# Kernel optimization log

Hardware: AMD Instinct MI355X
Metric: run time of the kernel (lower is better)

Reference implementation:

```python
import jax, jax.numpy as jnp
import numpy as np

N_NODES = 50000
NEG_SLOPE = 0.2


def _gat_conv(x, edge_index, W, att_src, att_dst, bias, heads, out_ch, concat):
    """PyG-style GATConv (add_self_loops=True, negative_slope=0.2).
    x: [N, F_in], edge_index: [2, E] (row=src, row=dst), W: [F_in, heads*out_ch],
    att_src/att_dst: [heads, out_ch], bias: [heads*out_ch] or [out_ch]."""
    N = x.shape[0]
    # add self-loops
    loops = jnp.arange(N, dtype=edge_index.dtype)
    src = jnp.concatenate([edge_index[0], loops])
    dst = jnp.concatenate([edge_index[1], loops])

    h = (x @ W).reshape(N, heads, out_ch)                 # [N, H, C]
    a_src = jnp.einsum('nhc,hc->nh', h, att_src)          # [N, H]
    a_dst = jnp.einsum('nhc,hc->nh', h, att_dst)          # [N, H]

    e = a_src[src] + a_dst[dst]                           # [E', H]
    e = jnp.where(e >= 0, e, NEG_SLOPE * e)               # leaky_relu

    # segment softmax over incoming edges of each dst node
    e_max = jax.ops.segment_max(e, dst, num_segments=N)   # [N, H]
    e_max = jnp.where(jnp.isfinite(e_max), e_max, 0.0)
    ex = jnp.exp(e - e_max[dst])                          # [E', H]
    denom = jax.ops.segment_sum(ex, dst, num_segments=N)  # [N, H]
    alpha = ex / (denom[dst] + 1e-16)                     # [E', H]

    msg = alpha[:, :, None] * h[src]                      # [E', H, C]
    out = jax.ops.segment_sum(msg, dst, num_segments=N)   # [N, H, C]

    if concat:
        out = out.reshape(N, heads * out_ch)
    else:
        out = out.mean(axis=1)
    return out + bias


def setup_inputs() -> dict:
    key = jax.random.key(0)
    ks = jax.random.split(key, 12)
    F_in, hid, H1, C, H2 = 512, 8, 8, 40, 1
    x = jax.random.normal(ks[0], (N_NODES, F_in), dtype=jnp.float32)
    edge_index = jax.random.randint(ks[1], (2, 1600000), 0, N_NODES, dtype=jnp.int64)
    s1 = 1.0 / np.sqrt(F_in)
    s2 = 1.0 / np.sqrt(hid * H1)
    return {
        'x': x,
        'edge_index': edge_index,
        'W1': jax.random.normal(ks[2], (F_in, H1 * hid), dtype=jnp.float32) * s1,
        'att_src1': jax.random.normal(ks[3], (H1, hid), dtype=jnp.float32) * s2,
        'att_dst1': jax.random.normal(ks[4], (H1, hid), dtype=jnp.float32) * s2,
        'b1': jnp.zeros((H1 * hid,), dtype=jnp.float32),
        'W2': jax.random.normal(ks[5], (H1 * hid, H2 * C), dtype=jnp.float32) * s2,
        'att_src2': jax.random.normal(ks[6], (H2, C), dtype=jnp.float32) * 0.15,
        'att_dst2': jax.random.normal(ks[7], (H2, C), dtype=jnp.float32) * 0.15,
        'b2': jnp.zeros((C,), dtype=jnp.float32),
    }


def reference(x, edge_index, W1, att_src1, att_dst1, b1, W2, att_src2, att_dst2, b2):
    # eval mode: dropout is identity
    h = _gat_conv(x, edge_index, W1, att_src1, att_dst1, b1, heads=8, out_ch=8, concat=True)
    h = jax.nn.relu(h)
    h = _gat_conv(h, edge_index, W2, att_src2, att_dst2, b2, heads=1, out_ch=40, concat=False)
    return jax.nn.log_softmax(h, axis=1)
```

## Files before the change

### kernel.cpp

```cpp
#include <hip/hip_runtime.h>
#include <math.h>

#define NNODES 50000
#define NEG_SLOPE 0.2f
#define NB 391
#define BW 128
#define CHUNK 8192
#define CAP 8128

typedef __bf16 bf16x8 __attribute__((ext_vector_type(8)));
typedef float f32x4 __attribute__((ext_vector_type(4)));

__global__ void init_bcur(int* bcur) {
    int i = blockIdx.x * 256 + threadIdx.x;
    if (i < NB) bcur[i] = i * CAP;
    if (i == NB) bcur[NB] = 0;
}

__global__ __launch_bounds__(256) void bin_scatter(const int* __restrict__ ei,
                                                   int E, int N, int* bcur,
                                                   int* __restrict__ tmp) {
    __shared__ int lcnt[NB];
    __shared__ int lbase[NB];
    int tid = threadIdx.x;
    int base0 = blockIdx.x * CHUNK;
    int lim = min(base0 + CHUNK, E + N);
    for (int i = tid; i < NB; i += 256) lcnt[i] = 0;
    __syncthreads();
    for (int e = base0 + tid; e < lim; e += 256) {
        int d = (e < E) ? ei[E + e] : e - E;
        atomicAdd(&lcnt[d >> 7], 1);
    }
    __syncthreads();
    for (int b = tid; b < NB; b += 256) {
        int c = lcnt[b];
        lbase[b] = c ? atomicAdd(&bcur[b], c) : 0;
    }
    __syncthreads();
    for (int i = tid; i < NB; i += 256) lcnt[i] = 0;
    __syncthreads();
    for (int e = base0 + tid; e < lim; e += 256) {
        int s, d;
        if (e < E) { s = ei[e]; d = ei[E + e]; }
        else       { s = d = e - E; }
        int b = d >> 7;
        int p = atomicAdd(&lcnt[b], 1);
        tmp[lbase[b] + p] = ((d & 127) << 16) | s;
    }
}

__global__ __launch_bounds__(256) void csr_finalize(int* __restrict__ bcur,
                                                    const int* __restrict__ tmp,
                                                    int N, int* __restrict__ off,
                                                    int* __restrict__ off_end,
                                                    int* __restrict__ slot) {
    __shared__ int cnt[BW];
    __shared__ int cur[BW];
    __shared__ int cbase_s;
    int b = blockIdx.x, tid = threadIdx.x;
    int base = b * CAP;
    int m = bcur[b] - base;
    if (tid < BW) cnt[tid] = 0;
    __syncthreads();
    for (int i = tid; i < m; i += 256)
        atomicAdd(&cnt[(tmp[base + i] >> 16) & 127], 1);
    __syncthreads();
    if (tid == 0) cbase_s = atomicAdd(&bcur[NB], m);
    int myv = (tid < BW) ? cnt[tid] : 0;
    for (int o = 1; o < BW; o <<= 1) {
        int u = 0;
        if (tid >= o && tid < BW) u = cnt[tid - o];
        __syncthreads();
        if (tid < BW) cnt[tid] += u;
        __syncthreads();
    }
    if (tid < BW) {
        int ex = cbase_s + cnt[tid] - myv;
        cur[tid] = ex;
        int g = b * BW + tid;
        if (g < N) { off[g] = ex; off_end[g] = ex + myv; }
    }
    __syncthreads();
    for (int i = tid; i < m; i += 256) {
        int v = tmp[base + i];
        int k = (v >> 16) & 127;
        int p = atomicAdd(&cur[k], 1);
        slot[p] = v & 0xFFFF;
    }
}

__global__ void prep_w1(const float* __restrict__ W1, __bf16* __restrict__ W1b) {
    int i = blockIdx.x * 256 + threadIdx.x;
    if (i >= 512 * 64) return;
    int k = i >> 6, n = i & 63;
    W1b[((size_t)(k >> 3) * 64 + n) * 8 + (k & 7)] = (__bf16)W1[i];
}

__global__ __launch_bounds__(256) void gemm1_mfma(const float* __restrict__ X,
                                                  const __bf16* __restrict__ W1b,
                                                  __bf16* __restrict__ H1b, int M) {
    __shared__ __bf16 As[2048];
    __shared__ __bf16 Bs[2048];
    int tid = threadIdx.x, wid = tid >> 6, lane = tid & 63;
    int quad = lane >> 4, l15 = lane & 15;
    int m0 = blockIdx.x * 64;
    f32x4 acc[4] = {{0.f, 0.f, 0.f, 0.f}, {0.f, 0.f, 0.f, 0.f},
                    {0.f, 0.f, 0.f, 0.f}, {0.f, 0.f, 0.f, 0.f}};
    int mrow = tid >> 2;
    int kq_w = tid & 3;
    int xrow = min(m0 + mrow, M - 1);
    const float* xp = X + (size_t)xrow * 512 + kq_w * 8;
    for (int kb = 0; kb < 16; ++kb) {
        float4 xa = *(const float4*)(xp + kb * 32);
        float4 xb = *(const float4*)(xp + kb * 32 + 4);
        bf16x8 av;
        av[0] = (__bf16)xa.x; av[1] = (__bf16)xa.y;
        av[2] = (__bf16)xa.z; av[3] = (__bf16)xa.w;
        av[4] = (__bf16)xb.x; av[5] = (__bf16)xb.y;
        av[6] = (__bf16)xb.z; av[7] = (__bf16)xb.w;
        *(bf16x8*)(As + ((size_t)kq_w * 64 + mrow) * 8) = av;
        *(bf16x8*)(Bs + ((size_t)wid * 64 + lane) * 8) =
            *(const bf16x8*)(W1b + ((size_t)(kb * 4 + wid) * 64 + lane) * 8);
        __syncthreads();
        bf16x8 af = *(const bf16x8*)(As + ((size_t)quad * 64 + 16 * wid + l15) * 8);
#pragma unroll
        for (int t = 0; t < 4; ++t) {
            bf16x8 bf = *(const bf16x8*)(Bs + ((size_t)quad * 64 + 16 * t + l15) * 8);
            acc[t] = __builtin_amdgcn_mfma_f32_16x16x32_bf16(af, bf, acc[t], 0, 0, 0);
        }
        __syncthreads();
    }
#pragma unroll
    for (int t = 0; t < 4; ++t) {
#pragma unroll
        for (int r = 0; r < 4; ++r) {
            int gm = m0 + 16 * wid + quad * 4 + r;
            if (gm < M) H1b[(size_t)gm * 64 + 16 * t + l15] = (__bf16)acc[t][r];
        }
    }
}

__global__ void att1_kernel(const __bf16* __restrict__ H1b,
                            const float* __restrict__ att_src,
                            const float* __restrict__ att_dst,
                            float* __restrict__ a_src, float* __restrict__ a_dst,
                            int N) {
    int idx = blockIdx.x * 256 + threadIdx.x;
    if (idx >= N * 8) return;
    int h = idx & 7;
    bf16x8 hv = *(const bf16x8*)(H1b + (size_t)idx * 8);
    const float* sp = att_src + h * 8;
    const float* dp = att_dst + h * 8;
    float as = 0.f, ad = 0.f;
#pragma unroll
    for (int j = 0; j < 8; ++j) {
        float hf = (float)hv[j];
        as += hf * sp[j];
        ad += hf * dp[j];
    }
    a_src[idx] = as;
    a_dst[idx] = ad;
}

__global__ __launch_bounds__(256) void agg1(const int* __restrict__ off,
                                            const int* __restrict__ off_end,
                                            const int* __restrict__ slot,
                                            const __bf16* __restrict__ H1b,
                                            const float* __restrict__ a_src,
                                            const float* __restrict__ a_dst,
                                            const float* __restrict__ b1,
                                            float* __restrict__ H1R) {
    int wid = threadIdx.x >> 6, lane = threadIdx.x & 63;
    int d = blockIdx.x * 4 + wid;
    int beg = off[d], end = off_end[d];
    int h = lane >> 3;
    int eh = lane & 7;
    int es = lane >> 3;
    float adst_c = a_dst[(size_t)d * 8 + eh];
    float acc = 0.f, den_l = 0.f;
    for (int i = beg; i < end; i += 8) {
        int j = i + es;
        int jj = (j < end) ? j : (end - 1);
        int s = slot[jj];
        float e = a_src[(size_t)s * 8 + eh] + adst_c;
        e = (e >= 0.f) ? e : NEG_SLOPE * e;
        float w = (j < end) ? __expf(e) : 0.f;
        den_l += w;
#pragma unroll
        for (int q = 0; q < 8; ++q) {
            int sq = __builtin_amdgcn_readlane(s, q << 3);
            float wq = __shfl(w, (q << 3) | h);
            acc += wq * (float)H1b[(size_t)sq * 64 + lane];
        }
    }
    den_l += __shfl_xor(den_l, 8);
    den_l += __shfl_xor(den_l, 16);
    den_l += __shfl_xor(den_l, 32);
    float den = __shfl(den_l, h);
    float v = acc / (den + 1e-16f) + b1[lane];
    H1R[(size_t)d * 64 + lane] = (v > 0.f) ? v : 0.f;
}

__global__ __launch_bounds__(256) void gemm2_att2(const float* __restrict__ H1R,
                                                  const float* __restrict__ W2,
                                                  const float* __restrict__ att_src2,
                                                  const float* __restrict__ att_dst2,
                                                  __bf16* __restrict__ H2b,
                                                  float* __restrict__ a_src2,
                                                  float* __restrict__ a_dst2) {
    __shared__ float W2s[64 * 40];
    __shared__ float rows[4][64];
    int tid = threadIdx.x;
    int wid = tid >> 6, lane = tid & 63;
    for (int i = tid; i < 64 * 40; i += 256) W2s[i] = W2[i];
    int node = blockIdx.x * 4 + wid;
    rows[wid][lane] = H1R[(size_t)node * 64 + lane];
    __syncthreads();
    int c = lane;
    int cc = (c < 40) ? c : 0;
    float acc = 0.f;
#pragma unroll 8
    for (int k = 0; k < 64; ++k) acc += rows[wid][k] * W2s[k * 40 + cc];
    if (c < 40) H2b[(size_t)node * 40 + c] = (__bf16)acc;
    float ps = (c < 40) ? acc * att_src2[c] : 0.f;
    float pd = (c < 40) ? acc * att_dst2[c] : 0.f;
#pragma unroll
    for (int m = 32; m >= 1; m >>= 1) {
        ps += __shfl_xor(ps, m);
        pd += __shfl_xor(pd, m);
    }
    if (lane == 0) { a_src2[node] = ps; a_dst2[node] = pd; }
}

__global__ __launch_bounds__(256) void agg2(const int* __restrict__ off,
                                            const int* __restrict__ off_end,
                                            const int* __restrict__ slot,
                                            const __bf16* __restrict__ H2b,
                                            const float* __restrict__ a_src2,
                                            const float* __restrict__ a_d2,
                                            const float* __restrict__ b2,
                                            float* __restrict__ out) {
    int wid = threadIdx.x >> 6, lane = threadIdx.x & 63;
    int d = blockIdx.x * 4 + wid;
    int beg = off[d], end = off_end[d];
    float adst = a_d2[d];
    int c = lane;
    int cc = (c < 40) ? c : 0;
    float acc = 0.f, den = 0.f;
    for (int i = beg; i < end; i += 64) {
        int j = i + lane;
        int jj = (j < end) ? j : (end - 1);
        int s = slot[jj];
        float e = a_src2[s] + adst;
        e = (e >= 0.f) ? e : NEG_SLOPE * e;
        float w = (j < end) ? __expf(e) : 0.f;
        den += w;
#pragma unroll
        for (int qb = 0; qb < 8; ++qb) {
            if (i + (qb << 3) >= end) break;
#pragma unroll
            for (int qq = 0; qq < 8; ++qq) {
                int q = (qb << 3) + qq;
                int sq = __builtin_amdgcn_readlane(s, q);
                float wq = __uint_as_float(
                    __builtin_amdgcn_readlane((int)__float_as_uint(w), q));
                acc += wq * (float)H2b[(size_t)sq * 40 + cc];
            }
        }
    }
#pragma unroll
    for (int m = 32; m >= 1; m >>= 1) den += __shfl_xor(den, m);
    float v = acc / (den + 1e-16f) + b2[cc];
    float vm = (c < 40) ? v : -3.0e38f;
#pragma unroll
    for (int m = 32; m >= 1; m >>= 1) vm = fmaxf(vm, __shfl_xor(vm, m));
    float se = (c < 40) ? __expf(v - vm) : 0.f;
#pragma unroll
    for (int m = 32; m >= 1; m >>= 1) se += __shfl_xor(se, m);
    float res = v - vm - __logf(se);
    if (c < 40) out[(size_t)d * 40 + c] = res;
}

extern "C" void kernel_launch(void* const* d_in, const int* in_sizes, int n_in,
                              void* d_out, int out_size, void* d_ws, size_t ws_size,
                              hipStream_t stream) {
    const float* x   = (const float*)d_in[0];
    const int*   ei  = (const int*)d_in[1];
    const float* W1  = (const float*)d_in[2];
    const float* as1 = (const float*)d_in[3];
    const float* ad1 = (const float*)d_in[4];
    const float* b1  = (const float*)d_in[5];
    const float* W2  = (const float*)d_in[6];
    const float* as2 = (const float*)d_in[7];
    const float* ad2 = (const float*)d_in[8];
    const float* b2  = (const float*)d_in[9];
    float* out = (float*)d_out;

    const int N = NNODES;
    const int E = in_sizes[1] / 2;
    const int total = E + N;

    char* ws = (char*)d_ws;
    size_t o = 0;
    auto alloc = [&](size_t bytes) -> void* {
        void* p = ws + o;
        o = (o + bytes + 255) & ~(size_t)255;
        return p;
    };
    int* bcur    = (int*)alloc((size_t)(NB + 1) * 4);
    int* off     = (int*)alloc((size_t)N * 4);
    int* off_end = (int*)alloc((size_t)N * 4);
    int* slot    = (int*)alloc((size_t)total * 4);
    __bf16* W1b = (__bf16*)alloc((size_t)512 * 64 * 2);
    __bf16* H1b = (__bf16*)alloc((size_t)N * 64 * 2);
    float* a_s1 = (float*)alloc((size_t)N * 8 * 4);
    float* a_d1 = (float*)alloc((size_t)N * 8 * 4);
    float* H1R  = (float*)alloc((size_t)N * 64 * 4);
    __bf16* H2b = (__bf16*)alloc((size_t)N * 40 * 2);
    float* a_s2 = (float*)alloc((size_t)N * 4);
    float* a_d2 = (float*)alloc((size_t)N * 4);
    int* tmp = (int*)H1R;
    (void)ws_size; (void)n_in; (void)out_size;

    init_bcur<<<(NB + 256) / 256, 256, 0, stream>>>(bcur);
    bin_scatter<<<(total + CHUNK - 1) / CHUNK, 256, 0, stream>>>(ei, E, N, bcur, tmp);
    csr_finalize<<<NB, 256, 0, stream>>>(bcur, tmp, N, off, off_end, slot);

    prep_w1<<<(512 * 64 + 255) / 256, 256, 0, stream>>>(W1, W1b);
    gemm1_mfma<<<(N + 63) / 64, 256, 0, stream>>>(x, W1b, H1b, N);
    att1_kernel<<<(N * 8 + 255) / 256, 256, 0, stream>>>(H1b, as1, ad1, a_s1, a_d1, N);
    agg1<<<N / 4, 256, 0, stream>>>(off, off_end, slot, H1b, a_s1, a_d1, b1, H1R);

    gemm2_att2<<<N / 4, 256, 0, stream>>>(H1R, W2, as2, ad2, H2b, a_s2, a_d2);
    agg2<<<N / 4, 256, 0, stream>>>(off, off_end, slot, H2b, a_s2, a_d2, b2, out);
}
```

Measured before the change: 363.2 us.

## Vectorize bf16 gathers in aggregation kernels and batch nodes in gemm2

agg1 and agg2 now read two bf16 features per lane with 32-bit loads, so each wavefront gathers several source rows at once (two edges per wave in agg1, three in agg2), with a cross-lane reduction at the end. gemm2_att2 handles 16 nodes per block and reads shared-memory rows as float4, so W2 is loaded into shared memory fewer times. The bin_scatter chunk size is halved to launch more blocks. The goal is fewer and wider gather instructions and better memory-level parallelism on the edge loops, at the cost of extra shuffles, and in agg2 four idle lanes per wave.

```diff
diff --git a/kernel.cpp b/kernel.cpp
--- a/kernel.cpp
+++ b/kernel.cpp
@@ -5,7 +5,7 @@
 #define NEG_SLOPE 0.2f
 #define NB 391
 #define BW 128
-#define CHUNK 8192
+#define CHUNK 4096
 #define CAP 8128
 
 typedef __bf16 bf16x8 __attribute__((ext_vector_type(8)));
@@ -173,11 +173,13 @@
     int wid = threadIdx.x >> 6, lane = threadIdx.x & 63;
     int d = blockIdx.x * 4 + wid;
     int beg = off[d], end = off_end[d];
-    int h = lane >> 3;
-    int eh = lane & 7;
-    int es = lane >> 3;
+    int es = lane >> 3, eh = lane & 7;
+    int half = lane >> 5;
+    int m = lane & 31;
+    int ghead = m >> 2;
     float adst_c = a_dst[(size_t)d * 8 + eh];
-    float acc = 0.f, den_l = 0.f;
+    float ax = 0.f, ay = 0.f, den_l = 0.f;
+    const unsigned short* H1u = (const unsigned short*)H1b;
     for (int i = beg; i < end; i += 8) {
         int j = i + es;
         int jj = (j < end) ? j : (end - 1);
@@ -187,18 +189,30 @@
         float w = (j < end) ? __expf(e) : 0.f;
         den_l += w;
 #pragma unroll
-        for (int q = 0; q < 8; ++q) {
-            int sq = __builtin_amdgcn_readlane(s, q << 3);
-            float wq = __shfl(w, (q << 3) | h);
-            acc += wq * (float)H1b[(size_t)sq * 64 + lane];
-        }
-    }
+        for (int q = 0; q < 4; ++q) {
+            int eidx = 2 * q + half;
+            int sE = __shfl(s, eidx << 3);
+            float wE = __shfl(w, (eidx << 3) | ghead);
+            unsigned hv = *(const unsigned*)(H1u + (size_t)sE * 64 + 2 * m);
+            ax += wE * __uint_as_float(hv << 16);
+            ay += wE * __uint_as_float(hv & 0xFFFF0000u);
+        }
+    }
+    ax += __shfl_xor(ax, 32);
+    ay += __shfl_xor(ay, 32);
     den_l += __shfl_xor(den_l, 8);
     den_l += __shfl_xor(den_l, 16);
     den_l += __shfl_xor(den_l, 32);
-    float den = __shfl(den_l, h);
-    float v = acc / (den + 1e-16f) + b1[lane];
-    H1R[(size_t)d * 64 + lane] = (v > 0.f) ? v : 0.f;
+    float den = __shfl(den_l, ghead);
+    float inv = 1.f / (den + 1e-16f);
+    if (lane < 32) {
+        float2 bv = *(const float2*)(b1 + 2 * m);
+        float v0 = ax * inv + bv.x;
+        float v1 = ay * inv + bv.y;
+        v0 = (v0 > 0.f) ? v0 : 0.f;
+        v1 = (v1 > 0.f) ? v1 : 0.f;
+        *(float2*)(H1R + (size_t)d * 64 + 2 * m) = make_float2(v0, v1);
+    }
 }
 
 __global__ __launch_bounds__(256) void gemm2_att2(const float* __restrict__ H1R,
@@ -209,27 +223,41 @@
                                                   float* __restrict__ a_src2,
                                                   float* __restrict__ a_dst2) {
     __shared__ float W2s[64 * 40];
-    __shared__ float rows[4][64];
+    __shared__ float rows[16][64];
     int tid = threadIdx.x;
     int wid = tid >> 6, lane = tid & 63;
     for (int i = tid; i < 64 * 40; i += 256) W2s[i] = W2[i];
-    int node = blockIdx.x * 4 + wid;
-    rows[wid][lane] = H1R[(size_t)node * 64 + lane];
+    int nb = blockIdx.x * 16;
+#pragma unroll
+    for (int r = 0; r < 4; ++r)
+        rows[r * 4 + wid][lane] = H1R[(size_t)(nb + r * 4 + wid) * 64 + lane];
     __syncthreads();
     int c = lane;
     int cc = (c < 40) ? c : 0;
-    float acc = 0.f;
-#pragma unroll 8
-    for (int k = 0; k < 64; ++k) acc += rows[wid][k] * W2s[k * 40 + cc];
-    if (c < 40) H2b[(size_t)node * 40 + c] = (__bf16)acc;
-    float ps = (c < 40) ? acc * att_src2[c] : 0.f;
-    float pd = (c < 40) ? acc * att_dst2[c] : 0.f;
-#pragma unroll
-    for (int m = 32; m >= 1; m >>= 1) {
-        ps += __shfl_xor(ps, m);
-        pd += __shfl_xor(pd, m);
-    }
-    if (lane == 0) { a_src2[node] = ps; a_dst2[node] = pd; }
+    float asc = att_src2[cc], adc = att_dst2[cc];
+#pragma unroll
+    for (int nn = 0; nn < 4; ++nn) {
+        int node = nb + wid * 4 + nn;
+        const float* rp = rows[wid * 4 + nn];
+        float acc = 0.f;
+#pragma unroll
+        for (int k4 = 0; k4 < 16; ++k4) {
+            float4 rv = *(const float4*)(rp + k4 * 4);
+            acc += rv.x * W2s[(k4 * 4 + 0) * 40 + cc];
+            acc += rv.y * W2s[(k4 * 4 + 1) * 40 + cc];
+            acc += rv.z * W2s[(k4 * 4 + 2) * 40 + cc];
+            acc += rv.w * W2s[(k4 * 4 + 3) * 40 + cc];
+        }
+        if (c < 40) H2b[(size_t)node * 40 + c] = (__bf16)acc;
+        float ps = (c < 40) ? acc * asc : 0.f;
+        float pd = (c < 40) ? acc * adc : 0.f;
+#pragma unroll
+        for (int mm = 32; mm >= 1; mm >>= 1) {
+            ps += __shfl_xor(ps, mm);
+            pd += __shfl_xor(pd, mm);
+        }
+        if (lane == 0) { a_src2[node] = ps; a_dst2[node] = pd; }
+    }
 }
 
 __global__ __launch_bounds__(256) void agg2(const int* __restrict__ off,
@@ -244,9 +272,10 @@
     int d = blockIdx.x * 4 + wid;
     int beg = off[d], end = off_end[d];
     float adst = a_d2[d];
-    int c = lane;
-    int cc = (c < 40) ? c : 0;
-    float acc = 0.f, den = 0.f;
+    int sub = lane / 20;
+    int part = lane % 20;
+    float ax = 0.f, ay = 0.f, den = 0.f;
+    const unsigned short* H2u = (const unsigned short*)H2b;
     for (int i = beg; i < end; i += 64) {
         int j = i + lane;
         int jj = (j < end) ? j : (end - 1);
@@ -256,27 +285,37 @@
         float w = (j < end) ? __expf(e) : 0.f;
         den += w;
 #pragma unroll
-        for (int qb = 0; qb < 8; ++qb) {
-            if (i + (qb << 3) >= end) break;
-#pragma unroll
-            for (int qq = 0; qq < 8; ++qq) {
-                int q = (qb << 3) + qq;
-                int sq = __builtin_amdgcn_readlane(s, q);
-                float wq = __uint_as_float(
-                    __builtin_amdgcn_readlane((int)__float_as_uint(w), q));
-                acc += wq * (float)H2b[(size_t)sq * 40 + cc];
-            }
-        }
-    }
-#pragma unroll
-    for (int m = 32; m >= 1; m >>= 1) den += __shfl_xor(den, m);
-    float v = acc / (den + 1e-16f) + b2[cc];
+        for (int g = 0; g < 22; ++g) {
+            if (i + g * 3 >= end) break;
+            int eidx = g * 3 + sub;
+            int el = (eidx < 64) ? eidx : 0;
+            int sE = __shfl(s, el);
+            float wE = __shfl(w, el);
+            if (sub == 3 || eidx >= 64) wE = 0.f;
+            unsigned hv = *(const unsigned*)(H2u + (size_t)sE * 40 + 2 * part);
+            ax += wE * __uint_as_float(hv << 16);
+            ay += wE * __uint_as_float(hv & 0xFFFF0000u);
+        }
+    }
+#pragma unroll
+    for (int mm = 32; mm >= 1; mm >>= 1) den += __shfl_xor(den, mm);
+    int c = lane;
+    int pc = (c < 40) ? (c >> 1) : 0;
+    float v = 0.f;
+#pragma unroll
+    for (int sb = 0; sb < 3; ++sb) {
+        float axs = __shfl(ax, sb * 20 + pc);
+        float ays = __shfl(ay, sb * 20 + pc);
+        v += (c & 1) ? ays : axs;
+    }
+    int cc = (c < 40) ? c : 0;
+    v = v / (den + 1e-16f) + b2[cc];
     float vm = (c < 40) ? v : -3.0e38f;
 #pragma unroll
-    for (int m = 32; m >= 1; m >>= 1) vm = fmaxf(vm, __shfl_xor(vm, m));
+    for (int mm = 32; mm >= 1; mm >>= 1) vm = fmaxf(vm, __shfl_xor(vm, mm));
     float se = (c < 40) ? __expf(v - vm) : 0.f;
 #pragma unroll
-    for (int m = 32; m >= 1; m >>= 1) se += __shfl_xor(se, m);
+    for (int mm = 32; mm >= 1; mm >>= 1) se += __shfl_xor(se, mm);
     float res = v - vm - __logf(se);
     if (c < 40) out[(size_t)d * 40 + c] = res;
 }
@@ -331,6 +370,6 @@
     att1_kernel<<<(N * 8 + 255) / 256, 256, 0, stream>>>(H1b, as1, ad1, a_s1, a_d1, N);
     agg1<<<N / 4, 256, 0, stream>>>(off, off_end, slot, H1b, a_s1, a_d1, b1, H1R);
 
-    gemm2_att2<<<N / 4, 256, 0, stream>>>(H1R, W2, as2, ad2, H2b, a_s2, a_d2);
+    gemm2_att2<<<N / 16, 256, 0, stream>>>(H1R, W2, as2, ad2, H2b, a_s2, a_d2);
     agg2<<<N / 4, 256, 0, stream>>>(off, off_end, slot, H2b, a_s2, a_d2, b2, out);
 }
```

After: 366.1 us. No clear change (+0.8%).

## Fuse layer-1 attention logits into GEMM1 and batch nodes in GEMM2

Applied to the files above, without the earlier changes.

Computes the layer-1 per-head attention logits inside the MFMA GEMM epilogue with shuffle reductions, which removes the separate att1 kernel and its re-read of H1. The layer-2 GEMM now handles 16 nodes per block instead of 4, so the W2 staging into shared memory is shared across more rows. The edge-binning chunk size is halved, giving more scatter blocks. Logits are now taken from fp32 accumulators rather than bf16-rounded values, a small numerical difference from before.

```diff
diff --git a/kernel.cpp b/kernel.cpp
--- a/kernel.cpp
+++ b/kernel.cpp
@@ -5,7 +5,7 @@
 #define NEG_SLOPE 0.2f
 #define NB 391
 #define BW 128
-#define CHUNK 8192
+#define CHUNK 4096
 #define CAP 8128
 
 typedef __bf16 bf16x8 __attribute__((ext_vector_type(8)));
@@ -98,7 +98,12 @@
 
 __global__ __launch_bounds__(256) void gemm1_mfma(const float* __restrict__ X,
                                                   const __bf16* __restrict__ W1b,
-                                                  __bf16* __restrict__ H1b, int M) {
+                                                  const float* __restrict__ att_s1,
+                                                  const float* __restrict__ att_d1,
+                                                  __bf16* __restrict__ H1b,
+                                                  float* __restrict__ a_s1,
+                                                  float* __restrict__ a_d1,
+                                                  int M) {
     __shared__ __bf16 As[2048];
     __shared__ __bf16 Bs[2048];
     int tid = threadIdx.x, wid = tid >> 6, lane = tid & 63;
@@ -130,36 +135,29 @@
         }
         __syncthreads();
     }
+    float asv[4], adv[4];
+#pragma unroll
+    for (int t = 0; t < 4; ++t) {
+        asv[t] = att_s1[16 * t + l15];
+        adv[t] = att_d1[16 * t + l15];
+    }
 #pragma unroll
     for (int t = 0; t < 4; ++t) {
 #pragma unroll
         for (int r = 0; r < 4; ++r) {
             int gm = m0 + 16 * wid + quad * 4 + r;
             if (gm < M) H1b[(size_t)gm * 64 + 16 * t + l15] = (__bf16)acc[t][r];
-        }
-    }
-}
-
-__global__ void att1_kernel(const __bf16* __restrict__ H1b,
-                            const float* __restrict__ att_src,
-                            const float* __restrict__ att_dst,
-                            float* __restrict__ a_src, float* __restrict__ a_dst,
-                            int N) {
-    int idx = blockIdx.x * 256 + threadIdx.x;
-    if (idx >= N * 8) return;
-    int h = idx & 7;
-    bf16x8 hv = *(const bf16x8*)(H1b + (size_t)idx * 8);
-    const float* sp = att_src + h * 8;
-    const float* dp = att_dst + h * 8;
-    float as = 0.f, ad = 0.f;
-#pragma unroll
-    for (int j = 0; j < 8; ++j) {
-        float hf = (float)hv[j];
-        as += hf * sp[j];
-        ad += hf * dp[j];
-    }
-    a_src[idx] = as;
-    a_dst[idx] = ad;
+            float ps = acc[t][r] * asv[t];
+            float pd = acc[t][r] * adv[t];
+            ps += __shfl_xor(ps, 1); ps += __shfl_xor(ps, 2); ps += __shfl_xor(ps, 4);
+            pd += __shfl_xor(pd, 1); pd += __shfl_xor(pd, 2); pd += __shfl_xor(pd, 4);
+            if (gm < M && (l15 & 7) == 0) {
+                int hh = 2 * t + (l15 >> 3);
+                a_s1[(size_t)gm * 8 + hh] = ps;
+                a_d1[(size_t)gm * 8 + hh] = pd;
+            }
+        }
+    }
 }
 
 __global__ __launch_bounds__(256) void agg1(const int* __restrict__ off,
@@ -209,27 +207,41 @@
                                                   float* __restrict__ a_src2,
                                                   float* __restrict__ a_dst2) {
     __shared__ float W2s[64 * 40];
-    __shared__ float rows[4][64];
+    __shared__ float rows[16][64];
     int tid = threadIdx.x;
     int wid = tid >> 6, lane = tid & 63;
     for (int i = tid; i < 64 * 40; i += 256) W2s[i] = W2[i];
-    int node = blockIdx.x * 4 + wid;
-    rows[wid][lane] = H1R[(size_t)node * 64 + lane];
+    int nb = blockIdx.x * 16;
+#pragma unroll
+    for (int r = 0; r < 4; ++r)
+        rows[r * 4 + wid][lane] = H1R[(size_t)(nb + r * 4 + wid) * 64 + lane];
     __syncthreads();
     int c = lane;
     int cc = (c < 40) ? c : 0;
-    float acc = 0.f;
-#pragma unroll 8
-    for (int k = 0; k < 64; ++k) acc += rows[wid][k] * W2s[k * 40 + cc];
-    if (c < 40) H2b[(size_t)node * 40 + c] = (__bf16)acc;
-    float ps = (c < 40) ? acc * att_src2[c] : 0.f;
-    float pd = (c < 40) ? acc * att_dst2[c] : 0.f;
-#pragma unroll
-    for (int m = 32; m >= 1; m >>= 1) {
-        ps += __shfl_xor(ps, m);
-        pd += __shfl_xor(pd, m);
-    }
-    if (lane == 0) { a_src2[node] = ps; a_dst2[node] = pd; }
+    float asc = att_src2[cc], adc = att_dst2[cc];
+#pragma unroll
+    for (int nn = 0; nn < 4; ++nn) {
+        int node = nb + wid * 4 + nn;
+        const float* rp = rows[wid * 4 + nn];
+        float acc = 0.f;
+#pragma unroll
+        for (int k4 = 0; k4 < 16; ++k4) {
+            float4 rv = *(const float4*)(rp + k4 * 4);
+            acc += rv.x * W2s[(k4 * 4 + 0) * 40 + cc];
+            acc += rv.y * W2s[(k4 * 4 + 1) * 40 + cc];
+            acc += rv.z * W2s[(k4 * 4 + 2) * 40 + cc];
+            acc += rv.w * W2s[(k4 * 4 + 3) * 40 + cc];
+        }
+        if (c < 40) H2b[(size_t)node * 40 + c] = (__bf16)acc;
+        float ps = (c < 40) ? acc * asc : 0.f;
+        float pd = (c < 40) ? acc * adc : 0.f;
+#pragma unroll
+        for (int mm = 32; mm >= 1; mm >>= 1) {
+            ps += __shfl_xor(ps, mm);
+            pd += __shfl_xor(pd, mm);
+        }
+        if (lane == 0) { a_src2[node] = ps; a_dst2[node] = pd; }
+    }
 }
 
 __global__ __launch_bounds__(256) void agg2(const int* __restrict__ off,
@@ -327,10 +339,9 @@
     csr_finalize<<<NB, 256, 0, stream>>>(bcur, tmp, N, off, off_end, slot);
 
     prep_w1<<<(512 * 64 + 255) / 256, 256, 0, stream>>>(W1, W1b);
-    gemm1_mfma<<<(N + 63) / 64, 256, 0, stream>>>(x, W1b, H1b, N);
-    att1_kernel<<<(N * 8 + 255) / 256, 256, 0, stream>>>(H1b, as1, ad1, a_s1, a_d1, N);
+    gemm1_mfma<<<(N + 63) / 64, 256, 0, stream>>>(x, W1b, as1, ad1, H1b, a_s1, a_d1, N);
     agg1<<<N / 4, 256, 0, stream>>>(off, off_end, slot, H1b, a_s1, a_d1, b1, H1R);
 
-    gemm2_att2<<<N / 4, 256, 0, stream>>>(H1R, W2, as2, ad2, H2b, a_s2, a_d2);
+    gemm2_att2<<<N / 16, 256, 0, stream>>>(H1R, W2, as2, ad2, H2b, a_s2, a_d2);
     agg2<<<N / 4, 256, 0, stream>>>(off, off_end, slot, H2b, a_s2, a_d2, b2, out);
 }
```

Measured after the change: 359.5 us. No clear change (-1.0%).
